# Kernel tuning notes

Measured on AMD Instinct MI355X. Metric: run time of the kernel, lower is better.

The kernel has to match this reference:

```python
import jax, jax.numpy as jnp
import numpy as np

BN_EPS = 1e-5

def bn(x, gamma, beta):
    # x: [N, C]; BatchNorm2d over (batch, spatial) == node axis here (training-mode batch stats)
    mu = x.mean(axis=0, keepdims=True)
    var = x.var(axis=0, keepdims=True)
    return (x - mu) * jax.lax.rsqrt(var + BN_EPS) * gamma + beta

def octree_conv(x, neigh, W):
    # x: [N, Cin]; neigh: [N, K] with values in [0, N], N == empty neighbor
    # W: [K, Cin, Cout]. Sparse octree conv = neighbor gather + contraction.
    xp = jnp.concatenate([x, jnp.zeros((1, x.shape[1]), x.dtype)], axis=0)  # zero row for empties
    g = xp[neigh]                                  # [N, K, Cin]
    return jnp.einsum('nkc,kcd->nd', g, W)         # [N, Cout]

def setup_inputs() -> dict:
    key = jax.random.key(0)
    ks = jax.random.split(key, 8)
    N, Cin, Cout, Cb, K = 60000, 256, 512, 128, 27
    s = 0.05
    return {
        'x': jax.random.normal(ks[0], (1, Cin, N, 1), jnp.float32),
        'neigh': jax.random.randint(ks[1], (N, K), 0, N + 1),
        'W1a': jax.random.normal(ks[2], (Cb, Cin), jnp.float32) * s,
        'g1a': jnp.ones((Cb,), jnp.float32), 'b1a': jnp.zeros((Cb,), jnp.float32),
        'W3': jax.random.normal(ks[3], (K, Cb, Cb), jnp.float32) * s,
        'g3': jnp.ones((Cb,), jnp.float32), 'b3': jnp.zeros((Cb,), jnp.float32),
        'W1b': jax.random.normal(ks[4], (Cout, Cb), jnp.float32) * s,
        'g1b': jnp.ones((Cout,), jnp.float32), 'b1b': jnp.zeros((Cout,), jnp.float32),
        'Wc': jax.random.normal(ks[5], (Cout, Cin), jnp.float32) * s,
        'gc': jnp.ones((Cout,), jnp.float32), 'bc': jnp.zeros((Cout,), jnp.float32),
    }

def reference(x, neigh, W1a, g1a, b1a, W3, g3, b3, W1b, g1b, b1b, Wc, gc, bc):
    h = jnp.squeeze(x, axis=(0, 3)).T                         # [N, Cin]
    c1 = jax.nn.relu(bn(h @ W1a.T, g1a, b1a))                 # 1x1 conv + BN + ReLU -> [N, Cb]
    c2 = jax.nn.relu(bn(octree_conv(c1, neigh, W3), g3, b3))  # sparse 3x3 octree conv + BN + ReLU
    c3 = bn(c2 @ W1b.T, g1b, b1b)                             # 1x1 conv + BN -> [N, Cout]
    sc = bn(h @ Wc.T, gc, bc)                                 # shortcut 1x1 conv + BN (Cin != Cout)
    out = jax.nn.relu(c3 + sc)
    return out.T[None, :, :, None]                            # [1, Cout, N, 1]
```

## Files before the change

### kernel.cpp

```cpp
#include <hip/hip_runtime.h>


typedef __bf16 bf16x8 __attribute__((ext_vector_type(8)));
typedef float f32x4 __attribute__((ext_vector_type(4)));
typedef unsigned short u16x8 __attribute__((ext_vector_type(8)));

__device__ __forceinline__ unsigned short f2bfu(float f) {
  union { float f; unsigned u; } v; v.f = f;
  unsigned r = v.u + 0x7fffu + ((v.u >> 16) & 1u);
  return (unsigned short)(r >> 16);
}
__device__ __forceinline__ float bfu2f(unsigned short s) {
  union { unsigned u; float f; } v; v.u = ((unsigned)s) << 16;
  return v.f;
}

__device__ __forceinline__ void gload_lds16(const unsigned short* g, unsigned short* l) {
  __builtin_amdgcn_global_load_lds(
      (const __attribute__((address_space(1))) unsigned int*)(unsigned long long)g,
      (__attribute__((address_space(3))) unsigned int*)(unsigned int)(unsigned long long)l,
      16, 0, 0);
}

__global__ __launch_bounds__(256) void prep_weights(
    const float* __restrict__ W1a, const float* __restrict__ W3,
    const float* __restrict__ W1b, const float* __restrict__ Wc,
    unsigned short* __restrict__ w1a, unsigned short* __restrict__ w3t,
    unsigned short* __restrict__ w1b, unsigned short* __restrict__ wc) {
  int i = blockIdx.x * 256 + threadIdx.x;
  int stride = gridDim.x * 256;
  for (; i < 442368; i += stride) {
    if (i < 32768)  w1a[i] = f2bfu(W1a[i]);
    if (i < 65536)  w1b[i] = f2bfu(W1b[i]);
    if (i < 131072) wc[i]  = f2bfu(Wc[i]);
    int k = i >> 14, rr = i & 16383;
    int d = rr >> 7, c = rr & 127;
    w3t[i] = f2bfu(W3[(k << 14) + (c << 7) + d]);
  }
}

__global__ __launch_bounds__(256) void transpose_x(
    const float* __restrict__ x, unsigned short* __restrict__ h, int M) {
  __shared__ float tile[64][65];
  int n0 = blockIdx.x * 64, c0 = blockIdx.y * 64;
  int t = threadIdx.x;
  int nl = t & 63;
#pragma unroll
  for (int i = 0; i < 16; ++i) {
    int cl = i * 4 + (t >> 6);
    int n = n0 + nl;
    tile[cl][nl] = (n < M) ? x[(size_t)(c0 + cl) * M + n] : 0.f;
  }
  __syncthreads();
  int cl = t & 63;
#pragma unroll
  for (int i = 0; i < 16; ++i) {
    int nl2 = i * 4 + (t >> 6);
    int n = n0 + nl2;
    h[(size_t)n * 256 + c0 + cl] = f2bfu(tile[cl][nl2]);
  }
}

__global__ __launch_bounds__(256) void gemm128(
    const unsigned short* __restrict__ A, const unsigned short* __restrict__ W,
    unsigned short* __restrict__ C, float* __restrict__ partials,
    int M, int Kd, int Nc) {
  __shared__ unsigned short sA[2][128 * 64];
  __shared__ unsigned short sB[2][128 * 64];
  __shared__ float sStat[4][2][128];
  int t = threadIdx.x, wave = t >> 6, lane = t & 63;
  int n0 = blockIdx.x * 128, m0 = blockIdx.y * 128;
  int wr = wave >> 1, wcc = wave & 1;
  int l4 = lane >> 4, lc = lane & 15, lc7 = lc & 7;
  int lrow = lane >> 3, lch = lane & 7;
  f32x4 acc[4][4] = {};
  const int np = Kd >> 6;

  auto STAGE = [&](int p, int buf) {
    int k0 = p << 6;
#pragma unroll
    for (int i = 0; i < 4; ++i) {
      int row = wave * 32 + i * 8 + lrow;
      int sc = lch ^ (row & 7);
      gload_lds16(A + (size_t)(m0 + row) * Kd + k0 + sc * 8, &sA[buf][(wave * 32 + i * 8) * 64]);
    }
#pragma unroll
    for (int i = 0; i < 4; ++i) {
      int row = wave * 32 + i * 8 + lrow;
      int sc = lch ^ (row & 7);
      gload_lds16(W + (size_t)(n0 + row) * Kd + k0 + sc * 8, &sB[buf][(wave * 32 + i * 8) * 64]);
    }
  };
  auto COMPUTE = [&](int buf) {
#pragma unroll
    for (int kk = 0; kk < 2; ++kk) {
      bf16x8 af[4], bfr[4];
#pragma unroll
      for (int mi = 0; mi < 4; ++mi) {
        int row = wr * 64 + mi * 16 + lc;
        int chunk = (kk * 4 + l4) ^ lc7;
        af[mi] = __builtin_bit_cast(bf16x8, *(const u16x8*)(&sA[buf][row * 64 + chunk * 8]));
      }
#pragma unroll
      for (int ni = 0; ni < 4; ++ni) {
        int row = wcc * 64 + ni * 16 + lc;
        int chunk = (kk * 4 + l4) ^ lc7;
        bfr[ni] = __builtin_bit_cast(bf16x8, *(const u16x8*)(&sB[buf][row * 64 + chunk * 8]));
      }
#pragma unroll
      for (int mi = 0; mi < 4; ++mi)
#pragma unroll
        for (int ni = 0; ni < 4; ++ni)
          acc[mi][ni] = __builtin_amdgcn_mfma_f32_16x16x32_bf16(af[mi], bfr[ni], acc[mi][ni], 0, 0, 0);
    }
  };

  STAGE(0, 0);
  __syncthreads();
  int cur = 0;
  for (int p = 0; p < np - 1; ++p) {
    STAGE(p + 1, cur ^ 1);
    COMPUTE(cur);
    __syncthreads();
    cur ^= 1;
  }
  COMPUTE(cur);

#pragma unroll
  for (int ni = 0; ni < 4; ++ni) {
    float s = 0.f, q = 0.f;
    int col = wcc * 64 + ni * 16 + lc;
#pragma unroll
    for (int mi = 0; mi < 4; ++mi)
#pragma unroll
      for (int j = 0; j < 4; ++j) {
        int n = m0 + wr * 64 + mi * 16 + l4 * 4 + j;
        unsigned short u = f2bfu(acc[mi][ni][j]);
        if (n < M) C[(size_t)n * Nc + n0 + col] = u;
        float v = bfu2f(u);
        s += v; q += v * v;
      }
    s += __shfl_xor(s, 16); s += __shfl_xor(s, 32);
    q += __shfl_xor(q, 16); q += __shfl_xor(q, 32);
    if (lane < 16) {
      sStat[wave][0][col] = s;
      sStat[wave][1][col] = q;
    }
  }
  __syncthreads();
  if (t < 128) {
    int wcs = t >> 6;
    float s = sStat[wcs][0][t] + sStat[wcs + 2][0][t];
    float q = sStat[wcs][1][t] + sStat[wcs + 2][1][t];
    partials[(size_t)blockIdx.y * (2 * Nc) + n0 + t] = s;
    partials[(size_t)blockIdx.y * (2 * Nc) + Nc + n0 + t] = q;
  }
}

__global__ __launch_bounds__(256) void octree_gemm(
    const unsigned short* __restrict__ c1, const int* __restrict__ neigh,
    const unsigned short* __restrict__ w3t, unsigned short* __restrict__ c2p,
    float* __restrict__ partials, int M) {
  __shared__ unsigned short sA[2][128 * 64];
  __shared__ unsigned short sB[2][128 * 64];
  __shared__ unsigned short nidx[128 * 27];
  __shared__ float sStat[4][2][128];
  int t = threadIdx.x, wave = t >> 6, lane = t & 63;
  int m0 = blockIdx.x * 128;
  for (int i = t; i < 128 * 27; i += 256) {
    int row = i / 27;
    nidx[i] = (unsigned short)((m0 + row < M) ? neigh[(size_t)m0 * 27 + i] : M);
  }
  __syncthreads();

  int wr = wave >> 1, wcc = wave & 1;
  int l4 = lane >> 4, lc = lane & 15, lc7 = lc & 7;
  int lrow = lane >> 3, lch = lane & 7;
  f32x4 acc[4][4] = {};

  auto STAGE = [&](int p, int buf) {
    int k = p >> 1, c0 = (p & 1) << 6;
#pragma unroll
    for (int i = 0; i < 4; ++i) {
      int row = wave * 32 + i * 8 + lrow;
      int nr = nidx[row * 27 + k];
      int sc = lch ^ (row & 7);
      gload_lds16(c1 + ((size_t)nr << 7) + c0 + sc * 8, &sA[buf][(wave * 32 + i * 8) * 64]);
    }
    const unsigned short* wk = w3t + ((size_t)k << 14);
#pragma unroll
    for (int i = 0; i < 4; ++i) {
      int row = wave * 32 + i * 8 + lrow;
      int sc = lch ^ (row & 7);
      gload_lds16(wk + ((size_t)row << 7) + c0 + sc * 8, &sB[buf][(wave * 32 + i * 8) * 64]);
    }
  };
  auto COMPUTE = [&](int buf) {
#pragma unroll
    for (int kk = 0; kk < 2; ++kk) {
      bf16x8 af[4], bfr[4];
#pragma unroll
      for (int mi = 0; mi < 4; ++mi) {
        int row = wr * 64 + mi * 16 + lc;
        int chunk = (kk * 4 + l4) ^ lc7;
        af[mi] = __builtin_bit_cast(bf16x8, *(const u16x8*)(&sA[buf][row * 64 + chunk * 8]));
      }
#pragma unroll
      for (int ni = 0; ni < 4; ++ni) {
        int row = wcc * 64 + ni * 16 + lc;
        int chunk = (kk * 4 + l4) ^ lc7;
        bfr[ni] = __builtin_bit_cast(bf16x8, *(const u16x8*)(&sB[buf][row * 64 + chunk * 8]));
      }
#pragma unroll
      for (int mi = 0; mi < 4; ++mi)
#pragma unroll
        for (int ni = 0; ni < 4; ++ni)
          acc[mi][ni] = __builtin_amdgcn_mfma_f32_16x16x32_bf16(af[mi], bfr[ni], acc[mi][ni], 0, 0, 0);
    }
  };

  STAGE(0, 0);
  __syncthreads();
  int cur = 0;
  for (int p = 0; p < 53; ++p) {
    STAGE(p + 1, cur ^ 1);
    COMPUTE(cur);
    __syncthreads();
    cur ^= 1;
  }
  COMPUTE(cur);

#pragma unroll
  for (int ni = 0; ni < 4; ++ni) {
    float s = 0.f, q = 0.f;
    int col = wcc * 64 + ni * 16 + lc;
#pragma unroll
    for (int mi = 0; mi < 4; ++mi)
#pragma unroll
      for (int j = 0; j < 4; ++j) {
        int n = m0 + wr * 64 + mi * 16 + l4 * 4 + j;
        unsigned short u = f2bfu(acc[mi][ni][j]);
        if (n < M) c2p[(size_t)n * 128 + col] = u;
        float v = bfu2f(u);
        s += v; q += v * v;
      }
    s += __shfl_xor(s, 16); s += __shfl_xor(s, 32);
    q += __shfl_xor(q, 16); q += __shfl_xor(q, 32);
    if (lane < 16) {
      sStat[wave][0][col] = s;
      sStat[wave][1][col] = q;
    }
  }
  __syncthreads();
  if (t < 128) {
    int wcs = t >> 6;
    float s = sStat[wcs][0][t] + sStat[wcs + 2][0][t];
    float q = sStat[wcs][1][t] + sStat[wcs + 2][1][t];
    partials[(size_t)blockIdx.x * 256 + t] = s;
    partials[(size_t)blockIdx.x * 256 + 128 + t] = q;
  }
}

__global__ __launch_bounds__(256) void bn_finalize(
    const float* __restrict__ partials, int nb, int C, int M,
    const float* __restrict__ g, const float* __restrict__ bt,
    float* __restrict__ ss) {
  int c = blockIdx.x;
  int t = threadIdx.x;
  float s = 0.f, s2 = 0.f;
  for (int b = t; b < nb; b += 256) {
    s += partials[(size_t)b * 2 * C + c];
    s2 += partials[(size_t)b * 2 * C + C + c];
  }
#pragma unroll
  for (int off = 32; off >= 1; off >>= 1) {
    s += __shfl_xor(s, off);
    s2 += __shfl_xor(s2, off);
  }
  __shared__ float sh[4][2];
  int wave = t >> 6, lane = t & 63;
  if (lane == 0) { sh[wave][0] = s; sh[wave][1] = s2; }
  __syncthreads();
  if (t == 0) {
    s = sh[0][0] + sh[1][0] + sh[2][0] + sh[3][0];
    s2 = sh[0][1] + sh[1][1] + sh[2][1] + sh[3][1];
    float mean = s / (float)M;
    float var = s2 / (float)M - mean * mean;
    float sc = g[c] * rsqrtf(var + 1e-5f);
    ss[c] = sc;
    ss[C + c] = bt[c] - mean * sc;
  }
}

__global__ __launch_bounds__(256) void bnrelu(
    const unsigned short* __restrict__ P, const float* __restrict__ ss,
    unsigned short* __restrict__ Aout, int total, int total2, int Cmask) {
  int i = (blockIdx.x * 256 + threadIdx.x) * 8;
  if (i >= total2) return;
  u16x8 o = {0, 0, 0, 0, 0, 0, 0, 0};
  if (i < total) {
    u16x8 v = *(const u16x8*)(P + i);
    int c0 = i & Cmask;
    int C = Cmask + 1;
#pragma unroll
    for (int j = 0; j < 8; ++j) {
      float f = bfu2f(v[j]) * ss[c0 + j] + ss[C + c0 + j];
      o[j] = f2bfu(fmaxf(f, 0.f));
    }
  }
  *(u16x8*)(Aout + i) = o;
}

__global__ __launch_bounds__(256) void final_out(
    const unsigned short* __restrict__ c3p, const unsigned short* __restrict__ scp,
    const float* __restrict__ ss3, const float* __restrict__ sssc,
    float* __restrict__ out, int M) {
  __shared__ float tile[64][65];
  int n0 = blockIdx.x * 64, c0 = blockIdx.y * 64;
  int t = threadIdx.x;
  int cl = t & 63;
#pragma unroll
  for (int i = 0; i < 16; ++i) {
    int nl = i * 4 + (t >> 6);
    int n = n0 + nl;
    float v = 0.f;
    if (n < M) {
      int c = c0 + cl;
      float a = bfu2f(c3p[(size_t)n * 512 + c]) * ss3[c] + ss3[512 + c];
      float b = bfu2f(scp[(size_t)n * 512 + c]) * sssc[c] + sssc[512 + c];
      v = fmaxf(a + b, 0.f);
    }
    tile[nl][cl] = v;
  }
  __syncthreads();
  int nl = t & 63;
#pragma unroll
  for (int i = 0; i < 16; ++i) {
    int cl2 = i * 4 + (t >> 6);
    int n = n0 + nl;
    if (n < M) out[(size_t)(c0 + cl2) * M + n0 + nl] = tile[nl][cl2];
  }
}

extern "C" void kernel_launch(void* const* d_in, const int* in_sizes, int n_in,
                              void* d_out, int out_size, void* d_ws, size_t ws_size,
                              hipStream_t stream) {
  const float* x   = (const float*)d_in[0];
  const int* neigh = (const int*)d_in[1];
  const float* W1a = (const float*)d_in[2];
  const float* g1a = (const float*)d_in[3];
  const float* b1a = (const float*)d_in[4];
  const float* W3  = (const float*)d_in[5];
  const float* g3  = (const float*)d_in[6];
  const float* b3  = (const float*)d_in[7];
  const float* W1b = (const float*)d_in[8];
  const float* g1b = (const float*)d_in[9];
  const float* b1b = (const float*)d_in[10];
  const float* Wc  = (const float*)d_in[11];
  const float* gc  = (const float*)d_in[12];
  const float* bc  = (const float*)d_in[13];
  float* out = (float*)d_out;

  const int M = in_sizes[1] / 27;
  const int MT = (M + 63) / 64;
  const int MTO = (M + 127) / 128;

  char* ws = (char*)d_ws;
  unsigned short* h   = (unsigned short*)(ws + 0);
  unsigned short* wA  = (unsigned short*)(ws + 30736384);
  unsigned short* wP  = (unsigned short*)(ws + 46104576);
  unsigned short* c3p = (unsigned short*)(ws + 61464576);
  unsigned short* scp = (unsigned short*)(ws + 122904576);
  unsigned short* w1a = (unsigned short*)(ws + 184344576);
  unsigned short* w3t = (unsigned short*)(ws + 184410112);
  unsigned short* w1b = (unsigned short*)(ws + 185294848);
  unsigned short* wc  = (unsigned short*)(ws + 185425920);
  float* ss1  = (float*)(ws + 185688064);
  float* ss2  = (float*)(ws + 185692160);
  float* ss3  = (float*)(ws + 185696256);
  float* sssc = (float*)(ws + 185700352);

  float* part12 = (float*)c3p;
  float* part3  = (float*)scp;
  float* partsc = (float*)wP;

  prep_weights<<<1728, 256, 0, stream>>>(W1a, W3, W1b, Wc, w1a, w3t, w1b, wc);
  transpose_x<<<dim3(MT, 4), 256, 0, stream>>>(x, h, M);

  const int total = M * 128, total2 = (MT * 64) * 128;
  const int bnGrid = (total2 / 8 + 255) / 256;

  gemm128<<<dim3(1, MTO), 256, 0, stream>>>(h, w1a, wP, part12, M, 256, 128);
  bn_finalize<<<128, 256, 0, stream>>>(part12, MTO, 128, M, g1a, b1a, ss1);
  bnrelu<<<bnGrid, 256, 0, stream>>>(wP, ss1, wA, total, total2, 127);

  octree_gemm<<<MTO, 256, 0, stream>>>(wA, neigh, w3t, wP, part12, M);
  bn_finalize<<<128, 256, 0, stream>>>(part12, MTO, 128, M, g3, b3, ss2);
  bnrelu<<<bnGrid, 256, 0, stream>>>(wP, ss2, wA, total, total2, 127);

  gemm128<<<dim3(4, MTO), 256, 0, stream>>>(wA, w1b, c3p, part3, M, 128, 512);
  bn_finalize<<<512, 256, 0, stream>>>(part3, MTO, 512, M, g1b, b1b, ss3);

  gemm128<<<dim3(4, MTO), 256, 0, stream>>>(h, wc, scp, partsc, M, 256, 512);
  bn_finalize<<<512, 256, 0, stream>>>(partsc, MTO, 512, M, gc, bc, sssc);

  final_out<<<dim3(MT, 8), 256, 0, stream>>>(c3p, scp, ss3, sssc, out, M);
}
```

Measured before the change: 266.1 us.

## Use 8 waves in octree gather-GEMM with explicit vmcnt pipelining and setprio

The octree conv GEMM now runs 512 threads (8 waves) per 128-row tile, with each wave owning 32x64 of the output instead of 64x64. The neighbor-index and stat shared buffers are unioned to save LDS. The main loop replaces __syncthreads with manual s_waitcnt vmcnt(4) plus s_barrier, so the next stage's gather loads can still be in flight while the current buffer is consumed. s_setprio raises priority around the MFMA block. More waves help hide gather latency, but each wave does less MFMA work per load and register and LDS pressure changes. The hand-set vmcnt value has to match the number of loads issued per stage.

Result: faster. 253.7 us (-4.7%).

```diff
diff --git a/kernel.cpp b/kernel.cpp
--- a/kernel.cpp
+++ b/kernel.cpp
@@ -157,51 +157,53 @@
   }
 }
 
-__global__ __launch_bounds__(256) void octree_gemm(
+__global__ __launch_bounds__(512, 4) void octree_gemm(
     const unsigned short* __restrict__ c1, const int* __restrict__ neigh,
     const unsigned short* __restrict__ w3t, unsigned short* __restrict__ c2p,
     float* __restrict__ partials, int M) {
   __shared__ unsigned short sA[2][128 * 64];
   __shared__ unsigned short sB[2][128 * 64];
-  __shared__ unsigned short nidx[128 * 27];
-  __shared__ float sStat[4][2][128];
+  __shared__ union {
+    unsigned short nidx[128 * 27];
+    float stat[8][2][128];
+  } u;
   int t = threadIdx.x, wave = t >> 6, lane = t & 63;
   int m0 = blockIdx.x * 128;
-  for (int i = t; i < 128 * 27; i += 256) {
+  for (int i = t; i < 128 * 27; i += 512) {
     int row = i / 27;
-    nidx[i] = (unsigned short)((m0 + row < M) ? neigh[(size_t)m0 * 27 + i] : M);
+    u.nidx[i] = (unsigned short)((m0 + row < M) ? neigh[(size_t)m0 * 27 + i] : M);
   }
   __syncthreads();
 
   int wr = wave >> 1, wcc = wave & 1;
   int l4 = lane >> 4, lc = lane & 15, lc7 = lc & 7;
   int lrow = lane >> 3, lch = lane & 7;
-  f32x4 acc[4][4] = {};
+  f32x4 acc[2][4] = {};
 
   auto STAGE = [&](int p, int buf) {
     int k = p >> 1, c0 = (p & 1) << 6;
 #pragma unroll
-    for (int i = 0; i < 4; ++i) {
-      int row = wave * 32 + i * 8 + lrow;
-      int nr = nidx[row * 27 + k];
+    for (int i = 0; i < 2; ++i) {
+      int row = wave * 16 + i * 8 + lrow;
+      int nr = u.nidx[row * 27 + k];
       int sc = lch ^ (row & 7);
-      gload_lds16(c1 + ((size_t)nr << 7) + c0 + sc * 8, &sA[buf][(wave * 32 + i * 8) * 64]);
+      gload_lds16(c1 + ((size_t)nr << 7) + c0 + sc * 8, &sA[buf][(wave * 16 + i * 8) * 64]);
     }
     const unsigned short* wk = w3t + ((size_t)k << 14);
 #pragma unroll
-    for (int i = 0; i < 4; ++i) {
-      int row = wave * 32 + i * 8 + lrow;
+    for (int i = 0; i < 2; ++i) {
+      int row = wave * 16 + i * 8 + lrow;
       int sc = lch ^ (row & 7);
-      gload_lds16(wk + ((size_t)row << 7) + c0 + sc * 8, &sB[buf][(wave * 32 + i * 8) * 64]);
+      gload_lds16(wk + ((size_t)row << 7) + c0 + sc * 8, &sB[buf][(wave * 16 + i * 8) * 64]);
     }
   };
   auto COMPUTE = [&](int buf) {
 #pragma unroll
     for (int kk = 0; kk < 2; ++kk) {
-      bf16x8 af[4], bfr[4];
-#pragma unroll
-      for (int mi = 0; mi < 4; ++mi) {
-        int row = wr * 64 + mi * 16 + lc;
+      bf16x8 af[2], bfr[4];
+#pragma unroll
+      for (int mi = 0; mi < 2; ++mi) {
+        int row = wr * 32 + mi * 16 + lc;
         int chunk = (kk * 4 + l4) ^ lc7;
         af[mi] = __builtin_bit_cast(bf16x8, *(const u16x8*)(&sA[buf][row * 64 + chunk * 8]));
       }
@@ -211,51 +213,63 @@
         int chunk = (kk * 4 + l4) ^ lc7;
         bfr[ni] = __builtin_bit_cast(bf16x8, *(const u16x8*)(&sB[buf][row * 64 + chunk * 8]));
       }
-#pragma unroll
-      for (int mi = 0; mi < 4; ++mi)
+      __builtin_amdgcn_s_setprio(1);
+#pragma unroll
+      for (int mi = 0; mi < 2; ++mi)
 #pragma unroll
         for (int ni = 0; ni < 4; ++ni)
           acc[mi][ni] = __builtin_amdgcn_mfma_f32_16x16x32_bf16(af[mi], bfr[ni], acc[mi][ni], 0, 0, 0);
+      __builtin_amdgcn_s_setprio(0);
     }
   };
 
   STAGE(0, 0);
-  __syncthreads();
-  int cur = 0;
-  for (int p = 0; p < 53; ++p) {
-    STAGE(p + 1, cur ^ 1);
+  for (int p = 0; p < 54; ++p) {
+    int cur = p & 1;
+    if (p < 53) {
+      STAGE(p + 1, cur ^ 1);
+      asm volatile("s_waitcnt vmcnt(4)" ::: "memory");
+    } else {
+      asm volatile("s_waitcnt vmcnt(0)" ::: "memory");
+    }
+    __builtin_amdgcn_sched_barrier(0);
+    __builtin_amdgcn_s_barrier();
+    __builtin_amdgcn_sched_barrier(0);
     COMPUTE(cur);
-    __syncthreads();
-    cur ^= 1;
-  }
-  COMPUTE(cur);
+    __builtin_amdgcn_sched_barrier(0);
+    __builtin_amdgcn_s_barrier();
+  }
 
 #pragma unroll
   for (int ni = 0; ni < 4; ++ni) {
     float s = 0.f, q = 0.f;
     int col = wcc * 64 + ni * 16 + lc;
 #pragma unroll
-    for (int mi = 0; mi < 4; ++mi)
+    for (int mi = 0; mi < 2; ++mi)
 #pragma unroll
       for (int j = 0; j < 4; ++j) {
-        int n = m0 + wr * 64 + mi * 16 + l4 * 4 + j;
-        unsigned short u = f2bfu(acc[mi][ni][j]);
-        if (n < M) c2p[(size_t)n * 128 + col] = u;
-        float v = bfu2f(u);
+        int n = m0 + wr * 32 + mi * 16 + l4 * 4 + j;
+        unsigned short uo = f2bfu(acc[mi][ni][j]);
+        if (n < M) c2p[(size_t)n * 128 + col] = uo;
+        float v = bfu2f(uo);
         s += v; q += v * v;
       }
     s += __shfl_xor(s, 16); s += __shfl_xor(s, 32);
     q += __shfl_xor(q, 16); q += __shfl_xor(q, 32);
     if (lane < 16) {
-      sStat[wave][0][col] = s;
-      sStat[wave][1][col] = q;
+      u.stat[wave][0][col] = s;
+      u.stat[wave][1][col] = q;
     }
   }
   __syncthreads();
   if (t < 128) {
     int wcs = t >> 6;
-    float s = sStat[wcs][0][t] + sStat[wcs + 2][0][t];
-    float q = sStat[wcs][1][t] + sStat[wcs + 2][1][t];
+    float s = 0.f, q = 0.f;
+#pragma unroll
+    for (int g = 0; g < 4; ++g) {
+      s += u.stat[g * 2 + wcs][0][t];
+      q += u.stat[g * 2 + wcs][1][t];
+    }
     partials[(size_t)blockIdx.x * 256 + t] = s;
     partials[(size_t)blockIdx.x * 256 + 128 + t] = q;
   }
@@ -394,7 +408,7 @@
   bn_finalize<<<128, 256, 0, stream>>>(part12, MTO, 128, M, g1a, b1a, ss1);
   bnrelu<<<bnGrid, 256, 0, stream>>>(wP, ss1, wA, total, total2, 127);
 
-  octree_gemm<<<MTO, 256, 0, stream>>>(wA, neigh, w3t, wP, part12, M);
+  octree_gemm<<<MTO, 512, 0, stream>>>(wA, neigh, w3t, wP, part12, M);
   bn_finalize<<<128, 256, 0, stream>>>(part12, MTO, 128, M, g3, b3, ss2);
   bnrelu<<<bnGrid, 256, 0, stream>>>(wP, ss2, wA, total, total2, 127);
 
```
